# Performance work log

Measured on AMD Instinct MI355X. Metric: run time of the kernel, lower is better.

## Reference

```python
import jax, jax.numpy as jnp
import numpy as np

B, N_USERS, N_ITEMS, E, UF, IF = 1024, 1000, 1000, 128, 32, 32
IN_SIZE = E + UF + E + IF  # 320
EPS = 1e-12


def _gru_zero_hidden(x, w_ih, b_ih, b_hh):
    # PyTorch GRUCell with hx=None (zeros): h' = (1-z)*n
    gi = x @ w_ih.T + b_ih                      # (B, 3E)
    i_r, i_z, i_n = jnp.split(gi, 3, axis=1)
    h_r, h_z, h_n = jnp.split(b_hh, 3)
    r = jax.nn.sigmoid(i_r + h_r)
    z = jax.nn.sigmoid(i_z + h_z)
    n = jnp.tanh(i_n + r * h_n)
    return (1.0 - z) * n


def _l2_normalize(x):
    nrm = jnp.sqrt(jnp.sum(x * x, axis=1, keepdims=True))
    return x / jnp.maximum(nrm, EPS)


def setup_inputs() -> dict:
    key = jax.random.key(0)
    ks = jax.random.split(key, 10)
    uid = jax.random.randint(ks[0], (B,), 0, N_USERS)
    iid = jax.random.randint(ks[1], (B,), 0, N_ITEMS)
    feats = jax.random.normal(ks[2], (B, UF + IF), dtype=jnp.float32)
    inputs = jnp.concatenate([uid[:, None].astype(jnp.float32), iid[:, None].astype(jnp.float32), feats], axis=1)
    s = 0.05
    return {
        "inputs": inputs,
        "user_memory": jax.random.normal(ks[3], (B, N_USERS, E), dtype=jnp.float32),
        "item_memory": jax.random.normal(ks[4], (B, N_ITEMS, E), dtype=jnp.float32),
        "w_ih_u": jax.random.normal(ks[5], (3 * E, IN_SIZE), dtype=jnp.float32) * s,
        "b_ih_u": jnp.zeros((3 * E,), dtype=jnp.float32),
        "b_hh_u": jnp.zeros((3 * E,), dtype=jnp.float32),
        "w_ih_i": jax.random.normal(ks[6], (3 * E, IN_SIZE), dtype=jnp.float32) * s,
        "b_ih_i": jnp.zeros((3 * E,), dtype=jnp.float32),
        "b_hh_i": jnp.zeros((3 * E,), dtype=jnp.float32),
    }


def reference(inputs, user_memory, item_memory, w_ih_u, b_ih_u, b_hh_u, w_ih_i, b_ih_i, b_hh_i):
    b = jnp.arange(B)
    user_ids = inputs[:, 0].astype(jnp.int32)
    item_ids = inputs[:, 1].astype(jnp.int32)
    user_features = inputs[:, 2:2 + UF]
    item_features = inputs[:, 2 + UF:]
    # gather per-batch-row memory slots
    um = user_memory[b, user_ids]               # (B, E)
    im = item_memory[b, item_ids]               # (B, E)
    user_inputs = jnp.concatenate([um, user_features, im, item_features], axis=1)
    item_inputs = jnp.concatenate([im, item_features, um, user_features], axis=1)
    new_u = _gru_zero_hidden(user_inputs, w_ih_u, b_ih_u, b_hh_u)
    new_i = _gru_zero_hidden(item_inputs, w_ih_i, b_ih_i, b_hh_i)
    new_u = _l2_normalize(new_u)
    new_i = _l2_normalize(new_i)
    # scatter back into memories
    user_memory = user_memory.at[b, user_ids].set(new_u)
    item_memory = item_memory.at[b, item_ids].set(new_i)
    out = jnp.concatenate([user_ids[:, None].astype(jnp.float32), item_ids[:, None].astype(jnp.float32), new_u, new_i], axis=1)
    return out, user_memory, item_memory
```

## Files before the change

kernel.cpp:

```cpp
#include <hip/hip_runtime.h>
#include <math.h>

#define BATCH 1024
#define NU 1000
#define NI 1000
#define EDIM 128
#define INROW 66
#define IN_SIZE 320
#define OUTROW 258
#define G 4
#define CHUNKS 5

typedef float f32x4 __attribute__((ext_vector_type(4)));

__global__ __launch_bounds__(256) void limnet_compute(
    const float* __restrict__ inputs,
    const float* __restrict__ umem,
    const float* __restrict__ imem,
    const float* __restrict__ w_u, const float* __restrict__ bih_u, const float* __restrict__ bhh_u,
    const float* __restrict__ w_i, const float* __restrict__ bih_i, const float* __restrict__ bhh_i,
    float* __restrict__ out)
{
    __shared__ float xx[G][640];
    __shared__ float gi[G][768];
    __shared__ float psum[4][G];
    __shared__ int   ids[G][2];

    const int t = threadIdx.x;
    const int wave = t >> 6, lane = t & 63;
    const int lane16 = lane & 15, sub = lane >> 4;
    const int b0 = blockIdx.x * G;

    for (int g = 0; g < G; ++g) {
        const int b = b0 + g;
        const float* inrow = inputs + (long)b * INROW;
        const int uid = (int)inrow[0];
        const int iid = (int)inrow[1];
        if (t == 0) { ids[g][0] = uid; ids[g][1] = iid; }
        if (t < 128) {
            float v = umem[((long)b * NU + uid) * EDIM + t];
            xx[g][t]       = v;  xx[g][320 + t] = v;
            float w = imem[((long)b * NI + iid) * EDIM + t];
            xx[g][160 + t] = w;  xx[g][480 + t] = w;
        } else {
            int s = t - 128;
            if (s < 32)      { float v = inrow[2 + s];  xx[g][128 + s] = v; xx[g][448 + s] = v; }
            else if (s < 64) { int s2 = s - 32; float v = inrow[34 + s2]; xx[g][288 + s2] = v; xx[g][608 + s2] = v; }
        }
    }
    __syncthreads();

    const int isItemW = (wave >= 2);
    const int xoff = isItemW ? 160 : 0;
    f32x4 xv[G][5];
    #pragma unroll
    for (int g = 0; g < G; ++g)
        #pragma unroll
        for (int i = 0; i < 5; ++i)
            xv[g][i] = *(const f32x4*)&xx[g][xoff + lane16 * 4 + i * 64];

    const float* wbase = isItemW ? w_i : w_u;
    const int rbase = (wave & 1) * 192;
    const int gibase = isItemW ? 384 : 0;
    for (int it = 0; it < 48; ++it) {
        const int row = rbase + it * 4 + sub;
        const float* wrow = wbase + (long)row * IN_SIZE;
        float acc[G] = {0.f, 0.f, 0.f, 0.f};
        #pragma unroll
        for (int i = 0; i < 5; ++i) {
            const f32x4 wv = *(const f32x4*)&wrow[lane16 * 4 + i * 64];
            #pragma unroll
            for (int g = 0; g < G; ++g)
                acc[g] += wv.x * xv[g][i].x + wv.y * xv[g][i].y
                        + wv.z * xv[g][i].z + wv.w * xv[g][i].w;
        }
        #pragma unroll
        for (int off = 8; off >= 1; off >>= 1) {
            #pragma unroll
            for (int g = 0; g < G; ++g) acc[g] += __shfl_xor(acc[g], off);
        }
        if (lane16 == 0) {
            #pragma unroll
            for (int g = 0; g < G; ++g) gi[g][gibase + row] = acc[g];
        }
    }
    __syncthreads();

    const int isItem = (t >= 128);
    const int d = isItem ? (t - 128) : t;
    const float* bih = isItem ? bih_i : bih_u;
    const float* bhh = isItem ? bhh_i : bhh_u;
    const float br = bih[d]       + bhh[d];
    const float bz = bih[128 + d] + bhh[128 + d];
    const float bn = bih[256 + d];
    const float hn = bhh[256 + d];
    const int gib = isItem ? 384 : 0;

    float val[G], ss[G];
    #pragma unroll
    for (int g = 0; g < G; ++g) {
        float ir  = gi[g][gib + d];
        float iz  = gi[g][gib + 128 + d];
        float inn = gi[g][gib + 256 + d];
        float r = 1.f / (1.f + expf(-(ir + br)));
        float z = 1.f / (1.f + expf(-(iz + bz)));
        float n = tanhf(inn + bn + r * hn);
        val[g] = (1.f - z) * n;
        ss[g]  = val[g] * val[g];
    }
    #pragma unroll
    for (int off = 32; off >= 1; off >>= 1) {
        #pragma unroll
        for (int g = 0; g < G; ++g) ss[g] += __shfl_xor(ss[g], off);
    }
    if (lane == 0) {
        #pragma unroll
        for (int g = 0; g < G; ++g) psum[wave][g] = ss[g];
    }
    __syncthreads();

    #pragma unroll
    for (int g = 0; g < G; ++g) {
        float s = isItem ? (psum[2][g] + psum[3][g]) : (psum[0][g] + psum[1][g]);
        float denom = fmaxf(sqrtf(s), 1e-12f);
        float nv = val[g] / denom;
        out[(long)(b0 + g) * OUTROW + 2 + (isItem ? 128 : 0) + d] = nv;
    }
    if (t < 2 * G) {
        int g = t >> 1, col = t & 1;
        out[(long)(b0 + g) * OUTROW + col] = (float)ids[g][col];
    }
}

__global__ __launch_bounds__(256) void limnet_copy(
    const float* __restrict__ umem,
    const float* __restrict__ imem,
    const float* __restrict__ inputs,
    const float* __restrict__ outbase,
    float* __restrict__ udst,
    float* __restrict__ idst)
{
    const int item = blockIdx.y;
    const int b = blockIdx.x / CHUNKS;
    const int c = blockIdx.x - b * CHUNKS;
    const int t = threadIdx.x;

    const f32x4* __restrict__ src4 = (const f32x4*)(item ? imem : umem);
    f32x4* __restrict__ dst4 = (f32x4*)(item ? idst : udst);
    const int id = (int)inputs[(long)b * INROW + item];
    const float* __restrict__ newrow = outbase + (long)b * OUTROW + 2 + item * EDIM;

    const long bbase4 = (long)b * (NU * EDIM / 4);
    const int  cbase4 = c * 6400;

    #pragma unroll 5
    for (int i = 0; i < 25; ++i) {
        const int idx4 = cbase4 + i * 256 + t;
        const long g4 = bbase4 + idx4;
        f32x4 v = __builtin_nontemporal_load(&src4[g4]);
        if ((idx4 >> 5) == id) {
            const int o = (idx4 & 31) * 4;
            f32x4 nv = { newrow[o], newrow[o + 1], newrow[o + 2], newrow[o + 3] };
            v = nv;
        }
        __builtin_nontemporal_store(v, &dst4[g4]);
    }
}

extern "C" void kernel_launch(void* const* d_in, const int* in_sizes, int n_in,
                              void* d_out, int out_size, void* d_ws, size_t ws_size,
                              hipStream_t stream) {
    const float* inputs = (const float*)d_in[0];
    const float* umem   = (const float*)d_in[1];
    const float* imem   = (const float*)d_in[2];
    const float* w_u    = (const float*)d_in[3];
    const float* bih_u  = (const float*)d_in[4];
    const float* bhh_u  = (const float*)d_in[5];
    const float* w_i    = (const float*)d_in[6];
    const float* bih_i  = (const float*)d_in[7];
    const float* bhh_i  = (const float*)d_in[8];
    float* out = (float*)d_out;

    limnet_compute<<<BATCH / G, 256, 0, stream>>>(
        inputs, umem, imem, w_u, bih_u, bhh_u, w_i, bih_i, bhh_i, out);

    const long OUTSEC = (long)BATCH * OUTROW;
    const long MEMSZ  = (long)BATCH * NU * EDIM;

    dim3 cgrid(BATCH * CHUNKS, 2);
    limnet_copy<<<cgrid, 256, 0, stream>>>(
        umem, imem, inputs, out, out + OUTSEC, out + OUTSEC + MEMSZ);
}
```

Baseline: 436.6 us.

## Copy memories first, then scatter updated rows from compute kernel

The memory copy now runs first as a plain streaming copy with no per-element id check and no dependency on compute output. The compute kernel runs afterwards and writes the normalized rows directly into the destination memories, overwriting the copied slots. This removes the compare/select and the scattered reads of new rows from the copy loop. The copy loads also change from nontemporal to regular loads. Correctness depends on the compute kernel running after the copy on the same stream.

```diff
diff --git a/kernel.cpp b/kernel.cpp
--- a/kernel.cpp
+++ b/kernel.cpp
@@ -9,9 +9,22 @@
 #define IN_SIZE 320
 #define OUTROW 258
 #define G 4
-#define CHUNKS 5
 
 typedef float f32x4 __attribute__((ext_vector_type(4)));
+
+__global__ __launch_bounds__(256) void limnet_stream_copy(
+    const f32x4* __restrict__ usrc, const f32x4* __restrict__ isrc,
+    f32x4* __restrict__ udst, f32x4* __restrict__ idst)
+{
+    const f32x4* __restrict__ src = blockIdx.y ? isrc : usrc;
+    f32x4* __restrict__ dst = blockIdx.y ? idst : udst;
+    long p = (long)blockIdx.x * 6400 + threadIdx.x;
+    #pragma unroll
+    for (int i = 0; i < 25; ++i, p += 256) {
+        f32x4 v = src[p];
+        __builtin_nontemporal_store(v, &dst[p]);
+    }
+}
 
 __global__ __launch_bounds__(256) void limnet_compute(
     const float* __restrict__ inputs,
@@ -19,7 +32,8 @@
     const float* __restrict__ imem,
     const float* __restrict__ w_u, const float* __restrict__ bih_u, const float* __restrict__ bhh_u,
     const float* __restrict__ w_i, const float* __restrict__ bih_i, const float* __restrict__ bhh_i,
-    float* __restrict__ out)
+    float* __restrict__ out,
+    float* __restrict__ udst, float* __restrict__ idst)
 {
     __shared__ float xx[G][640];
     __shared__ float gi[G][768];
@@ -124,46 +138,14 @@
         float s = isItem ? (psum[2][g] + psum[3][g]) : (psum[0][g] + psum[1][g]);
         float denom = fmaxf(sqrtf(s), 1e-12f);
         float nv = val[g] / denom;
-        out[(long)(b0 + g) * OUTROW + 2 + (isItem ? 128 : 0) + d] = nv;
+        const int b = b0 + g;
+        out[(long)b * OUTROW + 2 + (isItem ? 128 : 0) + d] = nv;
+        if (isItem) idst[((long)b * NI + ids[g][1]) * EDIM + d] = nv;
+        else        udst[((long)b * NU + ids[g][0]) * EDIM + d] = nv;
     }
     if (t < 2 * G) {
         int g = t >> 1, col = t & 1;
         out[(long)(b0 + g) * OUTROW + col] = (float)ids[g][col];
-    }
-}
-
-__global__ __launch_bounds__(256) void limnet_copy(
-    const float* __restrict__ umem,
-    const float* __restrict__ imem,
-    const float* __restrict__ inputs,
-    const float* __restrict__ outbase,
-    float* __restrict__ udst,
-    float* __restrict__ idst)
-{
-    const int item = blockIdx.y;
-    const int b = blockIdx.x / CHUNKS;
-    const int c = blockIdx.x - b * CHUNKS;
-    const int t = threadIdx.x;
-
-    const f32x4* __restrict__ src4 = (const f32x4*)(item ? imem : umem);
-    f32x4* __restrict__ dst4 = (f32x4*)(item ? idst : udst);
-    const int id = (int)inputs[(long)b * INROW + item];
-    const float* __restrict__ newrow = outbase + (long)b * OUTROW + 2 + item * EDIM;
-
-    const long bbase4 = (long)b * (NU * EDIM / 4);
-    const int  cbase4 = c * 6400;
-
-    #pragma unroll 5
-    for (int i = 0; i < 25; ++i) {
-        const int idx4 = cbase4 + i * 256 + t;
-        const long g4 = bbase4 + idx4;
-        f32x4 v = __builtin_nontemporal_load(&src4[g4]);
-        if ((idx4 >> 5) == id) {
-            const int o = (idx4 & 31) * 4;
-            f32x4 nv = { newrow[o], newrow[o + 1], newrow[o + 2], newrow[o + 3] };
-            v = nv;
-        }
-        __builtin_nontemporal_store(v, &dst4[g4]);
     }
 }
 
@@ -181,13 +163,16 @@
     const float* bhh_i  = (const float*)d_in[8];
     float* out = (float*)d_out;
 
-    limnet_compute<<<BATCH / G, 256, 0, stream>>>(
-        inputs, umem, imem, w_u, bih_u, bhh_u, w_i, bih_i, bhh_i, out);
-
     const long OUTSEC = (long)BATCH * OUTROW;
     const long MEMSZ  = (long)BATCH * NU * EDIM;
+    float* udst = out + OUTSEC;
+    float* idst = out + OUTSEC + MEMSZ;
 
-    dim3 cgrid(BATCH * CHUNKS, 2);
-    limnet_copy<<<cgrid, 256, 0, stream>>>(
-        umem, imem, inputs, out, out + OUTSEC, out + OUTSEC + MEMSZ);
+    dim3 cgrid(5120, 2);
+    limnet_stream_copy<<<cgrid, 256, 0, stream>>>(
+        (const f32x4*)umem, (const f32x4*)imem, (f32x4*)udst, (f32x4*)idst);
+
+    limnet_compute<<<BATCH / G, 256, 0, stream>>>(
+        inputs, umem, imem, w_u, bih_u, bhh_u, w_i, bih_i, bhh_i,
+        out, udst, idst);
 }
```

After: 451.4 us. 1.03x slower.
